# Optimization experiments

Measured on AMD Instinct MI355X. Metric: run time of the kernel, lower is better.

## Reference

```python
import jax, jax.numpy as jnp
import numpy as np

D = 128
N_DATA = 100000
N_TASK = 20000
E = 1000000


def _conv_params(key, d):
    ks = jax.random.split(key, 9)
    s = 1.0 / np.sqrt(d)
    return dict(
        Wmn=jax.random.uniform(ks[0], (d, d), jnp.float32, -s, s),
        bmn=jnp.zeros((d,), jnp.float32),
        Wme=jax.random.uniform(ks[1], (d, 1), jnp.float32, -1.0, 1.0),
        bme=jnp.zeros((d,), jnp.float32),
        Wgn=jax.random.uniform(ks[2], (d, d), jnp.float32, -s, s),
        bgn=jnp.zeros((d,), jnp.float32),
        Wge=jax.random.uniform(ks[3], (d, 1), jnp.float32, -1.0, 1.0),
        bge=jnp.zeros((d,), jnp.float32),
        bias=jnp.zeros((d,), jnp.float32),  # HeteConvLayer bias, zeros-init
    )


def setup_inputs() -> dict:
    key = jax.random.key(0)
    ks = jax.random.split(key, 12)
    inp = {
        'x_data': jax.random.normal(ks[0], (N_DATA, D), jnp.float32),
        'x_task': jax.random.normal(ks[1], (N_TASK, D), jnp.float32),
        'src_dt': jax.random.randint(ks[2], (E,), 0, N_DATA, jnp.int32),
        'dst_dt': jax.random.randint(ks[3], (E,), 0, N_TASK, jnp.int32),
        'ef_dt': jax.random.uniform(ks[4], (E, 1), jnp.float32),
        'src_td': jax.random.randint(ks[5], (E,), 0, N_TASK, jnp.int32),
        'dst_td': jax.random.randint(ks[6], (E,), 0, N_DATA, jnp.int32),
        'ef_td': jax.random.uniform(ks[7], (E, 1), jnp.float32),
    }
    # two separate HeteConvLayers (cfg.kg.hete=True)
    for name, k in (('dt', ks[8]), ('td', ks[9])):
        for pn, pv in _conv_params(k, D).items():
            inp[pn + '_' + name] = pv
    s = 1.0 / np.sqrt(D)
    inp['Ws_data'] = jax.random.uniform(ks[10], (D, D), jnp.float32, -s, s)
    inp['bs_data'] = jnp.zeros((D,), jnp.float32)
    inp['Ws_task'] = jax.random.uniform(ks[11], (D, D), jnp.float32, -s, s)
    inp['bs_task'] = jnp.zeros((D,), jnp.float32)
    return inp


def _hete_conv(x_neigh, src, dst, ef, Wmn, bmn, Wme, bme, Wgn, bgn, Wge, bge, bias, n_out):
    xj = x_neigh[src]                                   # [E, D] gather
    msg = xj @ Wmn.T + bmn + ef @ Wme.T + bme           # [E, D]
    gate = jax.nn.sigmoid(xj @ Wgn.T + bgn + ef @ Wge.T + bge) - 0.5  # gate_bias
    msg = msg * gate
    return jax.ops.segment_sum(msg, dst, num_segments=n_out) + bias


def _self_layer(x, Ws, bs):
    return (jax.nn.sigmoid(x @ Ws.T + bs) + 0.5) * x    # SelfLayer, gate_bias=True


def reference(x_data, x_task, src_dt, dst_dt, ef_dt, src_td, dst_td, ef_td,
              Wmn_dt, bmn_dt, Wme_dt, bme_dt, Wgn_dt, bgn_dt, Wge_dt, bge_dt, bias_dt,
              Wmn_td, bmn_td, Wme_td, bme_td, Wgn_td, bgn_td, Wge_td, bge_td, bias_td,
              Ws_data, bs_data, Ws_task, bs_task):
    # message type (data, property, task): neigh=data, self=task
    agg_task = _hete_conv(x_data, src_dt, dst_dt, ef_dt,
                          Wmn_dt, bmn_dt, Wme_dt, bme_dt,
                          Wgn_dt, bgn_dt, Wge_dt, bge_dt, bias_dt, N_TASK)
    # message type (task, property, data): neigh=task, self=data
    agg_data = _hete_conv(x_task, src_td, dst_td, ef_td,
                          Wmn_td, bmn_td, Wme_td, bme_td,
                          Wgn_td, bgn_td, Wge_td, bge_td, bias_td, N_DATA)
    # add self-transform, aggr='add', then Postlayer = ReLU
    data_emb = jax.nn.relu(agg_data + _self_layer(x_data, Ws_data, bs_data))
    task_emb = jax.nn.relu(agg_task + _self_layer(x_task, Ws_task, bs_task))
    # concatenate node-type outputs along node axis for a single output array
    return jnp.concatenate([data_emb, task_emb], axis=0)
```

## Files before the change

kernel.cpp:

```cpp
#include <hip/hip_runtime.h>
#include <hip/hip_bf16.h>
#include <cstdint>
#include <cstddef>

#define D_DIM 128
#define NEG_LOG2E (-1.44269504f)

typedef __attribute__((ext_vector_type(8))) short short8;
typedef __attribute__((ext_vector_type(4))) float f32x4;

__device__ __forceinline__ float sigmoid_fast(float z) {
  return __builtin_amdgcn_rcpf(1.0f + __expf(-z));
}

__device__ __forceinline__ unsigned short f2bf(float f) {
  union { float f; unsigned u; } v; v.f = f;
  unsigned r = v.u + 0x7FFF + ((v.u >> 16) & 1);
  return (unsigned short)(r >> 16);
}
__device__ __forceinline__ float bf_lo(unsigned u) { return __uint_as_float(u << 16); }
__device__ __forceinline__ float bf_hi(unsigned u) { return __uint_as_float(u & 0xFFFF0000u); }

__global__ __launch_bounds__(256) void fused_pre_kernel(
    const float* __restrict__ s0, const float* __restrict__ s1, const float* __restrict__ s2,
    const float* __restrict__ s3, const float* __restrict__ s4, const float* __restrict__ s5,
    short* __restrict__ wdst,
    const int* __restrict__ dst_dt, const int* __restrict__ dst_td,
    int* __restrict__ ghist, int* __restrict__ done,
    int* __restrict__ bbase, int* __restrict__ bcur, int* __restrict__ offsets,
    int nbt, int NB, int E, int n_tot) {
  __shared__ int lh[768];
  __shared__ int sc[256];
  __shared__ int lastflag;
  int t = threadIdx.x;

  if (blockIdx.x < 96) {
    int idx = blockIdx.x * 256 + t;
    int mat = idx >> 12;
    int pos = (idx & 4095) * 4;
    const float* s = (mat == 0) ? s0 : (mat == 1) ? s1 : (mat == 2) ? s2
                   : (mat == 3) ? s3 : (mat == 4) ? s4 : s5;
    float4 f = *(const float4*)(s + pos);
    short4 o;
    o.x = (short)f2bf(f.x); o.y = (short)f2bf(f.y);
    o.z = (short)f2bf(f.z); o.w = (short)f2bf(f.w);
    *(short4*)(wdst + mat * 16384 + pos) = o;
  }

  lh[t] = 0; lh[t + 256] = 0; lh[t + 512] = 0;
  __syncthreads();
  for (int i = blockIdx.x * 256 + t; i < E; i += gridDim.x * 256) {
    atomicAdd(&lh[dst_dt[i] >> 6], 1);
    atomicAdd(&lh[nbt + (dst_td[i] >> 8)], 1);
  }
  __syncthreads();
#pragma unroll
  for (int k = 0; k < 3; ++k) {
    int b = t + k * 256;
    int c = lh[b];
    if (b < NB && c) atomicAdd(&ghist[b], c);
  }
  __threadfence();
  __syncthreads();
  if (t == 0) {
    int prev = atomicAdd(done, 1);
    lastflag = (prev == (int)gridDim.x - 1);
  }
  __syncthreads();
  if (!lastflag) return;
  __threadfence();

  int i0 = t * 3;
  int c0 = (i0     < NB) ? atomicAdd(&ghist[i0],     0) : 0;
  int c1 = (i0 + 1 < NB) ? atomicAdd(&ghist[i0 + 1], 0) : 0;
  int c2 = (i0 + 2 < NB) ? atomicAdd(&ghist[i0 + 2], 0) : 0;
  int tot = c0 + c1 + c2;
  sc[t] = tot; __syncthreads();
  for (int s = 1; s < 256; s <<= 1) {
    int u = (t >= s) ? sc[t - s] : 0;
    __syncthreads(); sc[t] += u; __syncthreads();
  }
  int base = sc[t] - tot;
  if (i0     < NB) { bbase[i0]     = base;           bcur[i0]     = base; }
  if (i0 + 1 < NB) { bbase[i0 + 1] = base + c0;      bcur[i0 + 1] = base + c0; }
  if (i0 + 2 < NB) { bbase[i0 + 2] = base + c0 + c1; bcur[i0 + 2] = base + c0 + c1; }
  if (t == 255) { bbase[NB] = sc[255]; offsets[n_tot] = sc[255]; }
}

__global__ __launch_bounds__(256) void node_mfma_all(
    const float* __restrict__ x_data, const float* __restrict__ x_task,
    const short* __restrict__ Wb,
    const float* __restrict__ bmn_dt, const float* __restrict__ bme_dt,
    const float* __restrict__ bgn_dt, const float* __restrict__ bge_dt,
    const float* __restrict__ bmn_td, const float* __restrict__ bme_td,
    const float* __restrict__ bgn_td, const float* __restrict__ bge_td,
    const float* __restrict__ bs_data, const float* __restrict__ bs_task,
    const float* __restrict__ bias_dt, const float* __restrict__ bias_td,
    unsigned int* __restrict__ YG_dt, unsigned int* __restrict__ YG_td,
    float* __restrict__ out, int n_data, int n_task, int gd) {
  __shared__ unsigned sh[32][132];
  const bool is_data = (int)blockIdx.x < gd;
  const float* x; const short *Wmnb, *Wgnb, *Wsb;
  const float *bmn, *bme, *bgn, *bge, *bs, *bias_other;
  unsigned* YG; float* out_init; int n, bid;
  if (is_data) {
    x = x_data; Wmnb = Wb; Wgnb = Wb + 16384; Wsb = Wb + 32768;
    bmn = bmn_dt; bme = bme_dt; bgn = bgn_dt; bge = bge_dt;
    bs = bs_data; bias_other = bias_td;
    YG = YG_dt; out_init = out; n = n_data; bid = blockIdx.x;
  } else {
    x = x_task; Wmnb = Wb + 3 * 16384; Wgnb = Wb + 4 * 16384; Wsb = Wb + 5 * 16384;
    bmn = bmn_td; bme = bme_td; bgn = bgn_td; bge = bge_td;
    bs = bs_task; bias_other = bias_dt;
    YG = YG_td; out_init = out + (size_t)n_data * D_DIM; n = n_task; bid = blockIdx.x - gd;
  }
  const int t = threadIdx.x;
  const int wave = t >> 6, lane = t & 63;
  const int q = lane >> 4, l15 = lane & 15;
  const int ng = wave >> 1;
  const int h = (wave & 1) * 64;
  const int base_node = bid * 32;
  const int node_base = base_node + ng * 16;

  short8 a[4];
  {
    int m = node_base + l15;
    int mc = m < n ? m : (n - 1);
    const float* xrow = x + (size_t)mc * D_DIM;
#pragma unroll
    for (int ks = 0; ks < 4; ++ks) {
      float4 f0 = *(const float4*)(xrow + ks * 32 + q * 8);
      float4 f1 = *(const float4*)(xrow + ks * 32 + q * 8 + 4);
      union { short8 s; __hip_bfloat162 hh[4]; } u;
      u.hh[0] = __float22bfloat162_rn({f0.x, f0.y});
      u.hh[1] = __float22bfloat162_rn({f0.z, f0.w});
      u.hh[2] = __float22bfloat162_rn({f1.x, f1.y});
      u.hh[3] = __float22bfloat162_rn({f1.z, f1.w});
      a[ks] = u.s;
    }
  }

  f32x4 accY[4], accG[4], accS[4];
#pragma unroll
  for (int nt = 0; nt < 4; ++nt) { accY[nt] = {0,0,0,0}; accG[nt] = {0,0,0,0}; accS[nt] = {0,0,0,0}; }

#pragma unroll
  for (int nt = 0; nt < 4; ++nt) {
    const int row = h + nt * 16 + l15;
#pragma unroll
    for (int ks = 0; ks < 4; ++ks) {
      const int off = row * D_DIM + ks * 32 + q * 8;
      short8 bm  = *(const short8*)(Wmnb + off);
      short8 bg  = *(const short8*)(Wgnb + off);
      short8 bsw = *(const short8*)(Wsb + off);
      accY[nt] = __builtin_amdgcn_mfma_f32_16x16x32_bf16(a[ks], bm,  accY[nt], 0, 0, 0);
      accG[nt] = __builtin_amdgcn_mfma_f32_16x16x32_bf16(a[ks], bg,  accG[nt], 0, 0, 0);
      accS[nt] = __builtin_amdgcn_mfma_f32_16x16x32_bf16(a[ks], bsw, accS[nt], 0, 0, 0);
    }
  }

#pragma unroll
  for (int nt = 0; nt < 4; ++nt) {
    int d = h + nt * 16 + l15;
    float bmv = bmn[d] + bme[d];
    float bgv = bgn[d] + bge[d];
#pragma unroll
    for (int r = 0; r < 4; ++r) {
      union { __hip_bfloat162 hh; unsigned u; } pck;
      pck.hh = __float22bfloat162_rn({accY[nt][r] + bmv,
                                      (accG[nt][r] + bgv) * NEG_LOG2E});
      sh[ng * 16 + q * 4 + r][d] = pck.u;
    }
  }
  __syncthreads();
#pragma unroll
  for (int it = 0; it < 4; ++it) {
    int idx = (it * 256 + t) * 4;
    int nl = idx >> 7, dd = idx & 127;
    int node = base_node + nl;
    if (node < n)
      *(uint4*)(YG + (size_t)node * D_DIM + dd) = *(const uint4*)&sh[nl][dd];
  }
  __syncthreads();

  float* shf = (float*)sh;
#pragma unroll
  for (int nt = 0; nt < 4; ++nt) {
    int d = h + nt * 16 + l15;
    float bsv = bs[d];
#pragma unroll
    for (int r = 0; r < 4; ++r)
      shf[(ng * 16 + q * 4 + r) * 132 + d] = sigmoid_fast(accS[nt][r] + bsv) + 0.5f;
  }
  __syncthreads();
#pragma unroll
  for (int it = 0; it < 4; ++it) {
    int idx = (it * 256 + t) * 4;
    int nl = idx >> 7, dd = idx & 127;
    int node = base_node + nl;
    if (node < n) {
      float4 xv = *(const float4*)(x + (size_t)node * D_DIM + dd);
      float4 bo = *(const float4*)(bias_other + dd);
      const float* sp = &shf[nl * 132 + dd];
      float4 o;
      o.x = sp[0] * xv.x + bo.x;
      o.y = sp[1] * xv.y + bo.y;
      o.z = sp[2] * xv.z + bo.z;
      o.w = sp[3] * xv.w + bo.w;
      *(float4*)(out_init + (size_t)node * D_DIM + dd) = o;
    }
  }
}

__global__ __launch_bounds__(256) void sort_a_kernel(
    const int* __restrict__ src_dt, const int* __restrict__ dst_dt, const float* __restrict__ ef_dt,
    const int* __restrict__ src_td, const int* __restrict__ dst_td, const float* __restrict__ ef_td,
    int* __restrict__ bcur, int2* __restrict__ eA, int nbt, int NB, int E) {
  __shared__ int lh[768];
  __shared__ int lcur[768];
  int t = threadIdx.x;
  lh[t] = 0; lh[t + 256] = 0; lh[t + 512] = 0;
  __syncthreads();
  int e0 = blockIdx.x * 4096;
  int e1 = min(E, e0 + 4096);
  for (int i = e0 + t; i < e1; i += 256) {
    atomicAdd(&lh[dst_dt[i] >> 6], 1);
    atomicAdd(&lh[nbt + (dst_td[i] >> 8)], 1);
  }
  __syncthreads();
#pragma unroll
  for (int k = 0; k < 3; ++k) {
    int b = t + k * 256;
    int c = lh[b];
    if (b < NB && c) lcur[b] = atomicAdd(&bcur[b], c);
  }
  __syncthreads();
  for (int i = e0 + t; i < e1; i += 256) {
    int c = dst_dt[i];
    int bkt = c >> 6;
    int pos = atomicAdd(&lcur[bkt], 1);
    eA[pos] = make_int2(src_dt[i],
        (int)((__float_as_uint(ef_dt[i]) & 0xFFFFFF00u) | (unsigned)(c & 63)));
    int cd = dst_td[i];
    int bkt2 = nbt + (cd >> 8);
    int pos2 = atomicAdd(&lcur[bkt2], 1);
    eA[pos2] = make_int2(src_td[i],
        (int)((__float_as_uint(ef_td[i]) & 0xFFFFFF00u) | (unsigned)(cd & 255)));
  }
}

__global__ __launch_bounds__(256) void sort_b_kernel(
    const int2* __restrict__ eA, const int* __restrict__ bbase,
    int* __restrict__ offsets, int2* __restrict__ eB,
    int nbt, int n_task, int n_tot) {
  __shared__ int lh[256], sc[256], lcur[256];
  int b = blockIdx.x, t = threadIdx.x;
  int base = bbase[b];
  int cnt = bbase[b + 1] - base;
  int c0, nloc;
  if (b < nbt) { c0 = b << 6; nloc = min(64, n_task - c0); }
  else { c0 = n_task + ((b - nbt) << 8); nloc = min(256, n_tot - c0); }
  lh[t] = 0; __syncthreads();
  for (int i = base + t; i < base + cnt; i += 256)
    atomicAdd(&lh[((unsigned)eA[i].y) & 255u], 1);
  __syncthreads();
  int v = lh[t];
  sc[t] = v; __syncthreads();
  for (int s = 1; s < 256; s <<= 1) {
    int u = (t >= s) ? sc[t - s] : 0;
    __syncthreads(); sc[t] += u; __syncthreads();
  }
  int ex = sc[t] - v;
  lcur[t] = base + ex;
  if (t < nloc) offsets[c0 + t] = base + ex;
  __syncthreads();
  for (int i = base + t; i < base + cnt; i += 256) {
    int2 e = eA[i];
    int pos = atomicAdd(&lcur[((unsigned)e.y) & 255u], 1);
    eB[pos] = e;
  }
}

__device__ __forceinline__ void gstep(float2& acc, int2 e, const unsigned* __restrict__ YG,
                                      int lane, float2 wme, float2 wge2) {
  uint2 yg = *(const uint2*)(YG + (size_t)e.x * D_DIM + 2 * lane);
  float f = __int_as_float(e.y & (int)0xFFFFFF00);
  float g0 = __builtin_amdgcn_rcpf(1.0f + __builtin_amdgcn_exp2f(fmaf(f, wge2.x, bf_hi(yg.x)))) - 0.5f;
  float g1 = __builtin_amdgcn_rcpf(1.0f + __builtin_amdgcn_exp2f(fmaf(f, wge2.y, bf_hi(yg.y)))) - 0.5f;
  acc.x = fmaf(fmaf(f, wme.x, bf_lo(yg.x)), g0, acc.x);
  acc.y = fmaf(fmaf(f, wme.y, bf_lo(yg.y)), g1, acc.y);
}

__global__ __launch_bounds__(256) void gather_kernel(
    const unsigned* __restrict__ YG_dt, const unsigned* __restrict__ YG_td,
    const int* __restrict__ offsets, const int2* __restrict__ edata,
    const float* __restrict__ Wme_dt, const float* __restrict__ Wge_dt,
    const float* __restrict__ Wme_td, const float* __restrict__ Wge_td,
    float* __restrict__ out, int n_task, int n_data) {
  int w = (int)((blockIdx.x * 256u + threadIdx.x) >> 6);
  int lane = threadIdx.x & 63;
  if (w >= n_task + n_data) return;
  bool is_dt = w < n_task;
  const unsigned* YG = is_dt ? YG_dt : YG_td;
  const float* Wme = is_dt ? Wme_dt : Wme_td;
  const float* Wge = is_dt ? Wge_dt : Wge_td;
  size_t orow = is_dt ? (size_t)(n_data + w) : (size_t)(w - n_task);
  int beg = __builtin_amdgcn_readfirstlane(offsets[w]);
  int end = __builtin_amdgcn_readfirstlane(offsets[w + 1]);
  float2 wme = *(const float2*)(Wme + 2 * lane);
  float2 wge = *(const float2*)(Wge + 2 * lane);
  float2 wge2 = {wge.x * NEG_LOG2E, wge.y * NEG_LOG2E};
  float* op = out + orow * D_DIM + 2 * lane;
  float2 acc0 = *(const float2*)op;
  float2 acc1 = {0.0f, 0.0f};
  int p = beg;
  for (; p + 8 <= end; p += 8) {
    int2 e0 = edata[p],     e1 = edata[p + 1], e2 = edata[p + 2], e3 = edata[p + 3];
    int2 e4 = edata[p + 4], e5 = edata[p + 5], e6 = edata[p + 6], e7 = edata[p + 7];
    gstep(acc0, e0, YG, lane, wme, wge2);
    gstep(acc1, e1, YG, lane, wme, wge2);
    gstep(acc0, e2, YG, lane, wme, wge2);
    gstep(acc1, e3, YG, lane, wme, wge2);
    gstep(acc0, e4, YG, lane, wme, wge2);
    gstep(acc1, e5, YG, lane, wme, wge2);
    gstep(acc0, e6, YG, lane, wme, wge2);
    gstep(acc1, e7, YG, lane, wme, wge2);
  }
  for (; p + 2 <= end; p += 2) {
    int2 e0 = edata[p], e1 = edata[p + 1];
    gstep(acc0, e0, YG, lane, wme, wge2);
    gstep(acc1, e1, YG, lane, wme, wge2);
  }
  if (p < end) gstep(acc0, edata[p], YG, lane, wme, wge2);
  acc0.x = fmaxf(acc0.x + acc1.x, 0.0f);
  acc0.y = fmaxf(acc0.y + acc1.y, 0.0f);
  *(float2*)op = acc0;
}

extern "C" void kernel_launch(void* const* d_in, const int* in_sizes, int n_in,
                              void* d_out, int out_size, void* d_ws, size_t ws_size,
                              hipStream_t stream) {
  const float* x_data  = (const float*)d_in[0];
  const float* x_task  = (const float*)d_in[1];
  const int*   src_dt  = (const int*)d_in[2];
  const int*   dst_dt  = (const int*)d_in[3];
  const float* ef_dt   = (const float*)d_in[4];
  const int*   src_td  = (const int*)d_in[5];
  const int*   dst_td  = (const int*)d_in[6];
  const float* ef_td   = (const float*)d_in[7];
  const float* Wmn_dt  = (const float*)d_in[8];
  const float* bmn_dt  = (const float*)d_in[9];
  const float* Wme_dt  = (const float*)d_in[10];
  const float* bme_dt  = (const float*)d_in[11];
  const float* Wgn_dt  = (const float*)d_in[12];
  const float* bgn_dt  = (const float*)d_in[13];
  const float* Wge_dt  = (const float*)d_in[14];
  const float* bge_dt  = (const float*)d_in[15];
  const float* bias_dt = (const float*)d_in[16];
  const float* Wmn_td  = (const float*)d_in[17];
  const float* bmn_td  = (const float*)d_in[18];
  const float* Wme_td  = (const float*)d_in[19];
  const float* bme_td  = (const float*)d_in[20];
  const float* Wgn_td  = (const float*)d_in[21];
  const float* bgn_td  = (const float*)d_in[22];
  const float* Wge_td  = (const float*)d_in[23];
  const float* bge_td  = (const float*)d_in[24];
  const float* bias_td = (const float*)d_in[25];
  const float* Ws_data = (const float*)d_in[26];
  const float* bs_data = (const float*)d_in[27];
  const float* Ws_task = (const float*)d_in[28];
  const float* bs_task = (const float*)d_in[29];
  float* out = (float*)d_out;

  const int N_DATA = in_sizes[0] / D_DIM;
  const int N_TASK = in_sizes[1] / D_DIM;
  const int E = in_sizes[2];
  const int N_TOT = N_TASK + N_DATA;
  const int NBT = (N_TASK + 63) >> 6;
  const int NBD = (N_DATA + 255) >> 8;
  const int NB = NBT + NBD;
  const int GD = (N_DATA + 31) / 32;
  const int GT = (N_TASK + 31) / 32;

  char* ws = (char*)d_ws;
  size_t off = 0;
  auto alloc = [&](size_t bytes) { void* p = ws + off; off += (bytes + 255) & ~(size_t)255; return p; };
  unsigned int* YG_dt = (unsigned int*)alloc((size_t)N_DATA * D_DIM * 4);
  unsigned int* YG_td = (unsigned int*)alloc((size_t)N_TASK * D_DIM * 4);
  int2* eA     = (int2*)alloc((size_t)2 * E * 8);
  int2* eB     = (int2*)alloc((size_t)2 * E * 8);
  int*  offs   = (int*)alloc((size_t)(N_TOT + 1) * 4);
  int*  ghist  = (int*)alloc(1024 * 4);
  int*  bbase  = (int*)alloc(768 * 4);
  int*  bcur   = (int*)alloc(768 * 4);
  short* Wb    = (short*)alloc((size_t)6 * 16384 * 2);
  (void)ws_size; (void)n_in; (void)out_size;

  hipMemsetAsync(ghist, 0, 1024 * 4, stream);

  fused_pre_kernel<<<256, 256, 0, stream>>>(
      Wmn_dt, Wgn_dt, Ws_data, Wmn_td, Wgn_td, Ws_task, Wb,
      dst_dt, dst_td, ghist, ghist + 768, bbase, bcur, offs,
      NBT, NB, E, N_TOT);

  node_mfma_all<<<GD + GT, 256, 0, stream>>>(
      x_data, x_task, Wb,
      bmn_dt, bme_dt, bgn_dt, bge_dt,
      bmn_td, bme_td, bgn_td, bge_td,
      bs_data, bs_task, bias_dt, bias_td,
      YG_dt, YG_td, out, N_DATA, N_TASK, GD);

  sort_a_kernel<<<(E + 4095) / 4096, 256, 0, stream>>>(
      src_dt, dst_dt, ef_dt, src_td, dst_td, ef_td, bcur, eA, NBT, NB, E);
  sort_b_kernel<<<NB, 256, 0, stream>>>(eA, bbase, offs, eB, NBT, N_TASK, N_TOT);

  gather_kernel<<<(N_TOT + 3) / 4, 256, 0, stream>>>(
      YG_dt, YG_td, offs, eB, Wme_dt, Wge_dt, Wme_td, Wge_td, out, N_TASK, N_DATA);
}
```

Before: 492.0 us.

## Replace second sort pass with per-bucket LDS atomic accumulation gather

Drops the second counting-sort pass that ordered edges by exact destination node. Data-side buckets shrink from 256 to 64 nodes, and a new bucket-level gather kernel accumulates gated messages into a 64x128 LDS tile with shared-memory float atomics, then applies ReLU and writes out. This removes one full read and write of the edge array plus the per-node offsets, at the cost of many LDS atomics and a 32KB LDS footprint per block, which may limit occupancy.

```diff
diff --git a/kernel.cpp b/kernel.cpp
--- a/kernel.cpp
+++ b/kernel.cpp
@@ -27,9 +27,9 @@
     short* __restrict__ wdst,
     const int* __restrict__ dst_dt, const int* __restrict__ dst_td,
     int* __restrict__ ghist, int* __restrict__ done,
-    int* __restrict__ bbase, int* __restrict__ bcur, int* __restrict__ offsets,
-    int nbt, int NB, int E, int n_tot) {
-  __shared__ int lh[768];
+    int* __restrict__ bbase, int* __restrict__ bcur,
+    int nbt, int NB, int E) {
+  __shared__ int lh[2048];
   __shared__ int sc[256];
   __shared__ int lastflag;
   int t = threadIdx.x;
@@ -47,15 +47,16 @@
     *(short4*)(wdst + mat * 16384 + pos) = o;
   }
 
-  lh[t] = 0; lh[t + 256] = 0; lh[t + 512] = 0;
+#pragma unroll
+  for (int k = 0; k < 8; ++k) lh[t + k * 256] = 0;
   __syncthreads();
   for (int i = blockIdx.x * 256 + t; i < E; i += gridDim.x * 256) {
     atomicAdd(&lh[dst_dt[i] >> 6], 1);
-    atomicAdd(&lh[nbt + (dst_td[i] >> 8)], 1);
-  }
-  __syncthreads();
-#pragma unroll
-  for (int k = 0; k < 3; ++k) {
+    atomicAdd(&lh[nbt + (dst_td[i] >> 6)], 1);
+  }
+  __syncthreads();
+#pragma unroll
+  for (int k = 0; k < 8; ++k) {
     int b = t + k * 256;
     int c = lh[b];
     if (b < NB && c) atomicAdd(&ghist[b], c);
@@ -70,21 +71,24 @@
   if (!lastflag) return;
   __threadfence();
 
-  int i0 = t * 3;
-  int c0 = (i0     < NB) ? atomicAdd(&ghist[i0],     0) : 0;
-  int c1 = (i0 + 1 < NB) ? atomicAdd(&ghist[i0 + 1], 0) : 0;
-  int c2 = (i0 + 2 < NB) ? atomicAdd(&ghist[i0 + 2], 0) : 0;
-  int tot = c0 + c1 + c2;
-  sc[t] = tot; __syncthreads();
-  for (int s = 1; s < 256; s <<= 1) {
-    int u = (t >= s) ? sc[t - s] : 0;
+  int i0 = t * 8;
+  int c[8]; int s = 0;
+#pragma unroll
+  for (int k = 0; k < 8; ++k) {
+    c[k] = (i0 + k < NB) ? atomicAdd(&ghist[i0 + k], 0) : 0;
+    s += c[k];
+  }
+  sc[t] = s; __syncthreads();
+  for (int st = 1; st < 256; st <<= 1) {
+    int u = (t >= st) ? sc[t - st] : 0;
     __syncthreads(); sc[t] += u; __syncthreads();
   }
-  int base = sc[t] - tot;
-  if (i0     < NB) { bbase[i0]     = base;           bcur[i0]     = base; }
-  if (i0 + 1 < NB) { bbase[i0 + 1] = base + c0;      bcur[i0 + 1] = base + c0; }
-  if (i0 + 2 < NB) { bbase[i0 + 2] = base + c0 + c1; bcur[i0 + 2] = base + c0 + c1; }
-  if (t == 255) { bbase[NB] = sc[255]; offsets[n_tot] = sc[255]; }
+  int base = sc[t] - s;
+#pragma unroll
+  for (int k = 0; k < 8; ++k) {
+    if (i0 + k < NB) { bbase[i0 + k] = base; bcur[i0 + k] = base; base += c[k]; }
+  }
+  if (t == 255) bbase[NB] = sc[255];
 }
 
 __global__ __launch_bounds__(256) void node_mfma_all(
@@ -216,20 +220,21 @@
     const int* __restrict__ src_dt, const int* __restrict__ dst_dt, const float* __restrict__ ef_dt,
     const int* __restrict__ src_td, const int* __restrict__ dst_td, const float* __restrict__ ef_td,
     int* __restrict__ bcur, int2* __restrict__ eA, int nbt, int NB, int E) {
-  __shared__ int lh[768];
-  __shared__ int lcur[768];
+  __shared__ int lh[2048];
+  __shared__ int lcur[2048];
   int t = threadIdx.x;
-  lh[t] = 0; lh[t + 256] = 0; lh[t + 512] = 0;
+#pragma unroll
+  for (int k = 0; k < 8; ++k) lh[t + k * 256] = 0;
   __syncthreads();
   int e0 = blockIdx.x * 4096;
   int e1 = min(E, e0 + 4096);
   for (int i = e0 + t; i < e1; i += 256) {
     atomicAdd(&lh[dst_dt[i] >> 6], 1);
-    atomicAdd(&lh[nbt + (dst_td[i] >> 8)], 1);
-  }
-  __syncthreads();
-#pragma unroll
-  for (int k = 0; k < 3; ++k) {
+    atomicAdd(&lh[nbt + (dst_td[i] >> 6)], 1);
+  }
+  __syncthreads();
+#pragma unroll
+  for (int k = 0; k < 8; ++k) {
     int b = t + k * 256;
     int c = lh[b];
     if (b < NB && c) lcur[b] = atomicAdd(&bcur[b], c);
@@ -237,104 +242,72 @@
   __syncthreads();
   for (int i = e0 + t; i < e1; i += 256) {
     int c = dst_dt[i];
-    int bkt = c >> 6;
-    int pos = atomicAdd(&lcur[bkt], 1);
+    int pos = atomicAdd(&lcur[c >> 6], 1);
     eA[pos] = make_int2(src_dt[i],
         (int)((__float_as_uint(ef_dt[i]) & 0xFFFFFF00u) | (unsigned)(c & 63)));
     int cd = dst_td[i];
-    int bkt2 = nbt + (cd >> 8);
-    int pos2 = atomicAdd(&lcur[bkt2], 1);
+    int pos2 = atomicAdd(&lcur[nbt + (cd >> 6)], 1);
     eA[pos2] = make_int2(src_td[i],
-        (int)((__float_as_uint(ef_td[i]) & 0xFFFFFF00u) | (unsigned)(cd & 255)));
-  }
-}
-
-__global__ __launch_bounds__(256) void sort_b_kernel(
-    const int2* __restrict__ eA, const int* __restrict__ bbase,
-    int* __restrict__ offsets, int2* __restrict__ eB,
-    int nbt, int n_task, int n_tot) {
-  __shared__ int lh[256], sc[256], lcur[256];
-  int b = blockIdx.x, t = threadIdx.x;
-  int base = bbase[b];
-  int cnt = bbase[b + 1] - base;
-  int c0, nloc;
-  if (b < nbt) { c0 = b << 6; nloc = min(64, n_task - c0); }
-  else { c0 = n_task + ((b - nbt) << 8); nloc = min(256, n_tot - c0); }
-  lh[t] = 0; __syncthreads();
-  for (int i = base + t; i < base + cnt; i += 256)
-    atomicAdd(&lh[((unsigned)eA[i].y) & 255u], 1);
-  __syncthreads();
-  int v = lh[t];
-  sc[t] = v; __syncthreads();
-  for (int s = 1; s < 256; s <<= 1) {
-    int u = (t >= s) ? sc[t - s] : 0;
-    __syncthreads(); sc[t] += u; __syncthreads();
-  }
-  int ex = sc[t] - v;
-  lcur[t] = base + ex;
-  if (t < nloc) offsets[c0 + t] = base + ex;
-  __syncthreads();
-  for (int i = base + t; i < base + cnt; i += 256) {
-    int2 e = eA[i];
-    int pos = atomicAdd(&lcur[((unsigned)e.y) & 255u], 1);
-    eB[pos] = e;
-  }
-}
-
-__device__ __forceinline__ void gstep(float2& acc, int2 e, const unsigned* __restrict__ YG,
-                                      int lane, float2 wme, float2 wge2) {
-  uint2 yg = *(const uint2*)(YG + (size_t)e.x * D_DIM + 2 * lane);
-  float f = __int_as_float(e.y & (int)0xFFFFFF00);
-  float g0 = __builtin_amdgcn_rcpf(1.0f + __builtin_amdgcn_exp2f(fmaf(f, wge2.x, bf_hi(yg.x)))) - 0.5f;
-  float g1 = __builtin_amdgcn_rcpf(1.0f + __builtin_amdgcn_exp2f(fmaf(f, wge2.y, bf_hi(yg.y)))) - 0.5f;
-  acc.x = fmaf(fmaf(f, wme.x, bf_lo(yg.x)), g0, acc.x);
-  acc.y = fmaf(fmaf(f, wme.y, bf_lo(yg.y)), g1, acc.y);
-}
-
-__global__ __launch_bounds__(256) void gather_kernel(
+        (int)((__float_as_uint(ef_td[i]) & 0xFFFFFF00u) | (unsigned)(cd & 63)));
+  }
+}
+
+__global__ __launch_bounds__(256) void bucket_gather_kernel(
     const unsigned* __restrict__ YG_dt, const unsigned* __restrict__ YG_td,
-    const int* __restrict__ offsets, const int2* __restrict__ edata,
+    const int* __restrict__ bbase, const int2* __restrict__ eA,
     const float* __restrict__ Wme_dt, const float* __restrict__ Wge_dt,
     const float* __restrict__ Wme_td, const float* __restrict__ Wge_td,
-    float* __restrict__ out, int n_task, int n_data) {
-  int w = (int)((blockIdx.x * 256u + threadIdx.x) >> 6);
-  int lane = threadIdx.x & 63;
-  if (w >= n_task + n_data) return;
-  bool is_dt = w < n_task;
-  const unsigned* YG = is_dt ? YG_dt : YG_td;
-  const float* Wme = is_dt ? Wme_dt : Wme_td;
-  const float* Wge = is_dt ? Wge_dt : Wge_td;
-  size_t orow = is_dt ? (size_t)(n_data + w) : (size_t)(w - n_task);
-  int beg = __builtin_amdgcn_readfirstlane(offsets[w]);
-  int end = __builtin_amdgcn_readfirstlane(offsets[w + 1]);
+    float* __restrict__ out, int nbt, int n_task, int n_data) {
+  __shared__ float acc[64][D_DIM];
+  const int b = blockIdx.x, t = threadIdx.x;
+  const bool is_task = b < nbt;
+  const unsigned* YG = is_task ? YG_dt : YG_td;
+  const float* Wme = is_task ? Wme_dt : Wme_td;
+  const float* Wge = is_task ? Wge_dt : Wge_td;
+  int nloc; size_t orow0;
+  if (is_task) { int c0 = b << 6; nloc = min(64, n_task - c0); orow0 = (size_t)(n_data + c0); }
+  else         { int c0 = (b - nbt) << 6; nloc = min(64, n_data - c0); orow0 = (size_t)c0; }
+  float* outp = out + orow0 * D_DIM;
+  for (int i = t; i < (nloc << 5); i += 256) {
+    int r = i >> 5, cI = (i & 31) << 2;
+    *(float4*)&acc[r][cI] = *(const float4*)(outp + r * D_DIM + cI);
+  }
+  const int base = bbase[b], end = bbase[b + 1];
+  const int lane = t & 63, wave = t >> 6;
   float2 wme = *(const float2*)(Wme + 2 * lane);
   float2 wge = *(const float2*)(Wge + 2 * lane);
   float2 wge2 = {wge.x * NEG_LOG2E, wge.y * NEG_LOG2E};
-  float* op = out + orow * D_DIM + 2 * lane;
-  float2 acc0 = *(const float2*)op;
-  float2 acc1 = {0.0f, 0.0f};
-  int p = beg;
-  for (; p + 8 <= end; p += 8) {
-    int2 e0 = edata[p],     e1 = edata[p + 1], e2 = edata[p + 2], e3 = edata[p + 3];
-    int2 e4 = edata[p + 4], e5 = edata[p + 5], e6 = edata[p + 6], e7 = edata[p + 7];
-    gstep(acc0, e0, YG, lane, wme, wge2);
-    gstep(acc1, e1, YG, lane, wme, wge2);
-    gstep(acc0, e2, YG, lane, wme, wge2);
-    gstep(acc1, e3, YG, lane, wme, wge2);
-    gstep(acc0, e4, YG, lane, wme, wge2);
-    gstep(acc1, e5, YG, lane, wme, wge2);
-    gstep(acc0, e6, YG, lane, wme, wge2);
-    gstep(acc1, e7, YG, lane, wme, wge2);
-  }
-  for (; p + 2 <= end; p += 2) {
-    int2 e0 = edata[p], e1 = edata[p + 1];
-    gstep(acc0, e0, YG, lane, wme, wge2);
-    gstep(acc1, e1, YG, lane, wme, wge2);
-  }
-  if (p < end) gstep(acc0, edata[p], YG, lane, wme, wge2);
-  acc0.x = fmaxf(acc0.x + acc1.x, 0.0f);
-  acc0.y = fmaxf(acc0.y + acc1.y, 0.0f);
-  *(float2*)op = acc0;
+  __syncthreads();
+
+  for (int p = base + (wave << 3); p < end; p += 32) {
+    int lim = end - p; if (lim > 8) lim = 8;
+    int2 e[8];
+#pragma unroll
+    for (int j = 0; j < 8; ++j) if (j < lim) e[j] = eA[p + j];
+    uint2 yg[8];
+#pragma unroll
+    for (int j = 0; j < 8; ++j)
+      if (j < lim) yg[j] = *(const uint2*)(YG + (size_t)e[j].x * D_DIM + 2 * lane);
+#pragma unroll
+    for (int j = 0; j < 8; ++j) if (j < lim) {
+      float f = __int_as_float(e[j].y & (int)0xFFFFFF00);
+      float g0 = __builtin_amdgcn_rcpf(1.0f + __builtin_amdgcn_exp2f(fmaf(f, wge2.x, bf_hi(yg[j].x)))) - 0.5f;
+      float g1 = __builtin_amdgcn_rcpf(1.0f + __builtin_amdgcn_exp2f(fmaf(f, wge2.y, bf_hi(yg[j].y)))) - 0.5f;
+      float m0 = fmaf(f, wme.x, bf_lo(yg[j].x)) * g0;
+      float m1 = fmaf(f, wme.y, bf_lo(yg[j].y)) * g1;
+      int loc = e[j].y & 63;
+      atomicAdd(&acc[loc][2 * lane], m0);
+      atomicAdd(&acc[loc][2 * lane + 1], m1);
+    }
+  }
+  __syncthreads();
+  for (int i = t; i < (nloc << 5); i += 256) {
+    int r = i >> 5, cI = (i & 31) << 2;
+    float4 v = *(const float4*)&acc[r][cI];
+    v.x = fmaxf(v.x, 0.0f); v.y = fmaxf(v.y, 0.0f);
+    v.z = fmaxf(v.z, 0.0f); v.w = fmaxf(v.w, 0.0f);
+    *(float4*)(outp + r * D_DIM + cI) = v;
+  }
 }
 
 extern "C" void kernel_launch(void* const* d_in, const int* in_sizes, int n_in,
@@ -375,9 +348,8 @@
   const int N_DATA = in_sizes[0] / D_DIM;
   const int N_TASK = in_sizes[1] / D_DIM;
   const int E = in_sizes[2];
-  const int N_TOT = N_TASK + N_DATA;
   const int NBT = (N_TASK + 63) >> 6;
-  const int NBD = (N_DATA + 255) >> 8;
+  const int NBD = (N_DATA + 63) >> 6;
   const int NB = NBT + NBD;
   const int GD = (N_DATA + 31) / 32;
   const int GT = (N_TASK + 31) / 32;
@@ -388,20 +360,18 @@
   unsigned int* YG_dt = (unsigned int*)alloc((size_t)N_DATA * D_DIM * 4);
   unsigned int* YG_td = (unsigned int*)alloc((size_t)N_TASK * D_DIM * 4);
   int2* eA     = (int2*)alloc((size_t)2 * E * 8);
-  int2* eB     = (int2*)alloc((size_t)2 * E * 8);
-  int*  offs   = (int*)alloc((size_t)(N_TOT + 1) * 4);
-  int*  ghist  = (int*)alloc(1024 * 4);
-  int*  bbase  = (int*)alloc(768 * 4);
-  int*  bcur   = (int*)alloc(768 * 4);
+  int*  ghist  = (int*)alloc(2560 * 4);
+  int*  bbase  = (int*)alloc(2304 * 4);
+  int*  bcur   = (int*)alloc(2304 * 4);
   short* Wb    = (short*)alloc((size_t)6 * 16384 * 2);
   (void)ws_size; (void)n_in; (void)out_size;
 
-  hipMemsetAsync(ghist, 0, 1024 * 4, stream);
+  hipMemsetAsync(ghist, 0, 2560 * 4, stream);
 
   fused_pre_kernel<<<256, 256, 0, stream>>>(
       Wmn_dt, Wgn_dt, Ws_data, Wmn_td, Wgn_td, Ws_task, Wb,
-      dst_dt, dst_td, ghist, ghist + 768, bbase, bcur, offs,
-      NBT, NB, E, N_TOT);
+      dst_dt, dst_td, ghist, ghist + 2048, bbase, bcur,
+      NBT, NB, E);
 
   node_mfma_all<<<GD + GT, 256, 0, stream>>>(
       x_data, x_task, Wb,
@@ -412,8 +382,8 @@
 
   sort_a_kernel<<<(E + 4095) / 4096, 256, 0, stream>>>(
       src_dt, dst_dt, ef_dt, src_td, dst_td, ef_td, bcur, eA, NBT, NB, E);
-  sort_b_kernel<<<NB, 256, 0, stream>>>(eA, bbase, offs, eB, NBT, N_TASK, N_TOT);
-
-  gather_kernel<<<(N_TOT + 3) / 4, 256, 0, stream>>>(
-      YG_dt, YG_td, offs, eB, Wme_dt, Wge_dt, Wme_td, Wge_td, out, N_TASK, N_DATA);
-}
+
+  bucket_gather_kernel<<<NB, 256, 0, stream>>>(
+      YG_dt, YG_td, bbase, eA, Wme_dt, Wge_dt, Wme_td, Wge_td,
+      out, NBT, N_TASK, N_DATA);
+}
```

Measured after the change: 1.747 ms. +255.2%, slower.

## Replace two-pass bucket sort with per-node counting sort via global atomics

Applied to the files above, without the earlier changes.

Swaps the two-level bucketed edge sort (a coarse bucket histogram, a scatter into buckets, then a per-bucket local sort) for a direct per-destination counting sort. It builds a per-node histogram with global atomics, takes a three-kernel exclusive scan, and scatters edges with global atomic cursors. This drops the intermediate eA buffer and one full pass over the edges. In exchange it issues millions of global atomics, on contended counters for the task nodes (about 50 edges each), and it launches more kernels. The edge feature is now stored at full precision instead of carrying the low-byte destination index.

```diff
diff --git a/kernel.cpp b/kernel.cpp
--- a/kernel.cpp
+++ b/kernel.cpp
@@ -21,19 +21,13 @@
 __device__ __forceinline__ float bf_lo(unsigned u) { return __uint_as_float(u << 16); }
 __device__ __forceinline__ float bf_hi(unsigned u) { return __uint_as_float(u & 0xFFFF0000u); }
 
-__global__ __launch_bounds__(256) void fused_pre_kernel(
+__global__ __launch_bounds__(256) void wconv_hist_kernel(
     const float* __restrict__ s0, const float* __restrict__ s1, const float* __restrict__ s2,
     const float* __restrict__ s3, const float* __restrict__ s4, const float* __restrict__ s5,
     short* __restrict__ wdst,
     const int* __restrict__ dst_dt, const int* __restrict__ dst_td,
-    int* __restrict__ ghist, int* __restrict__ done,
-    int* __restrict__ bbase, int* __restrict__ bcur, int* __restrict__ offsets,
-    int nbt, int NB, int E, int n_tot) {
-  __shared__ int lh[768];
-  __shared__ int sc[256];
-  __shared__ int lastflag;
+    int* __restrict__ cnt, int n_task, int E) {
   int t = threadIdx.x;
-
   if (blockIdx.x < 96) {
     int idx = blockIdx.x * 256 + t;
     int mat = idx >> 12;
@@ -46,45 +40,69 @@
     o.z = (short)f2bf(f.z); o.w = (short)f2bf(f.w);
     *(short4*)(wdst + mat * 16384 + pos) = o;
   }
-
-  lh[t] = 0; lh[t + 256] = 0; lh[t + 512] = 0;
+  int E4 = E >> 2;
+  int i = blockIdx.x * 256 + t;
+  if (i < E4) {
+    int4 a = *(const int4*)(dst_dt + 4 * i);
+    atomicAdd(&cnt[a.x], 1); atomicAdd(&cnt[a.y], 1);
+    atomicAdd(&cnt[a.z], 1); atomicAdd(&cnt[a.w], 1);
+    int4 b = *(const int4*)(dst_td + 4 * i);
+    atomicAdd(&cnt[n_task + b.x], 1); atomicAdd(&cnt[n_task + b.y], 1);
+    atomicAdd(&cnt[n_task + b.z], 1); atomicAdd(&cnt[n_task + b.w], 1);
+  }
+  if (blockIdx.x == 0 && t < (E & 3)) {
+    int j = (E & ~3) + t;
+    atomicAdd(&cnt[dst_dt[j]], 1);
+    atomicAdd(&cnt[n_task + dst_td[j]], 1);
+  }
+}
+
+__global__ __launch_bounds__(256) void scan_p1_kernel(
+    const int* __restrict__ cnt, int* __restrict__ bsum, int n_tot) {
+  __shared__ int red[256];
+  int t = threadIdx.x;
+  int idx = blockIdx.x * 256 + t;
+  red[t] = (idx < n_tot) ? cnt[idx] : 0;
   __syncthreads();
-  for (int i = blockIdx.x * 256 + t; i < E; i += gridDim.x * 256) {
-    atomicAdd(&lh[dst_dt[i] >> 6], 1);
-    atomicAdd(&lh[nbt + (dst_td[i] >> 8)], 1);
-  }
-  __syncthreads();
-#pragma unroll
-  for (int k = 0; k < 3; ++k) {
-    int b = t + k * 256;
-    int c = lh[b];
-    if (b < NB && c) atomicAdd(&ghist[b], c);
-  }
-  __threadfence();
-  __syncthreads();
-  if (t == 0) {
-    int prev = atomicAdd(done, 1);
-    lastflag = (prev == (int)gridDim.x - 1);
-  }
-  __syncthreads();
-  if (!lastflag) return;
-  __threadfence();
-
-  int i0 = t * 3;
-  int c0 = (i0     < NB) ? atomicAdd(&ghist[i0],     0) : 0;
-  int c1 = (i0 + 1 < NB) ? atomicAdd(&ghist[i0 + 1], 0) : 0;
-  int c2 = (i0 + 2 < NB) ? atomicAdd(&ghist[i0 + 2], 0) : 0;
-  int tot = c0 + c1 + c2;
-  sc[t] = tot; __syncthreads();
+  for (int s = 128; s > 0; s >>= 1) {
+    if (t < s) red[t] += red[t + s];
+    __syncthreads();
+  }
+  if (t == 0) bsum[blockIdx.x] = red[0];
+}
+
+__global__ __launch_bounds__(512) void scan_p2_kernel(
+    const int* __restrict__ bsum, int* __restrict__ bpre,
+    int* __restrict__ offs, int SB, int n_tot) {
+  __shared__ int sc[512];
+  int t = threadIdx.x;
+  int v = (t < SB) ? bsum[t] : 0;
+  sc[t] = v; __syncthreads();
+  for (int s = 1; s < 512; s <<= 1) {
+    int u = (t >= s) ? sc[t - s] : 0;
+    __syncthreads(); sc[t] += u; __syncthreads();
+  }
+  if (t < SB) bpre[t] = sc[t] - v;
+  if (t == 511) offs[n_tot] = sc[511];
+}
+
+__global__ __launch_bounds__(256) void scan_p3_kernel(
+    const int* __restrict__ cnt, const int* __restrict__ bpre,
+    int* __restrict__ offs, int* __restrict__ cur, int n_tot) {
+  __shared__ int sc[256];
+  int t = threadIdx.x;
+  int idx = blockIdx.x * 256 + t;
+  int v = (idx < n_tot) ? cnt[idx] : 0;
+  sc[t] = v; __syncthreads();
   for (int s = 1; s < 256; s <<= 1) {
     int u = (t >= s) ? sc[t - s] : 0;
     __syncthreads(); sc[t] += u; __syncthreads();
   }
-  int base = sc[t] - tot;
-  if (i0     < NB) { bbase[i0]     = base;           bcur[i0]     = base; }
-  if (i0 + 1 < NB) { bbase[i0 + 1] = base + c0;      bcur[i0 + 1] = base + c0; }
-  if (i0 + 2 < NB) { bbase[i0 + 2] = base + c0 + c1; bcur[i0 + 2] = base + c0 + c1; }
-  if (t == 255) { bbase[NB] = sc[255]; offsets[n_tot] = sc[255]; }
+  if (idx < n_tot) {
+    int base = bpre[blockIdx.x] + sc[t] - v;
+    offs[idx] = base;
+    cur[idx] = base;
+  }
 }
 
 __global__ __launch_bounds__(256) void node_mfma_all(
@@ -212,79 +230,41 @@
   }
 }
 
-__global__ __launch_bounds__(256) void sort_a_kernel(
+__global__ __launch_bounds__(256) void scatter_kernel(
     const int* __restrict__ src_dt, const int* __restrict__ dst_dt, const float* __restrict__ ef_dt,
     const int* __restrict__ src_td, const int* __restrict__ dst_td, const float* __restrict__ ef_td,
-    int* __restrict__ bcur, int2* __restrict__ eA, int nbt, int NB, int E) {
-  __shared__ int lh[768];
-  __shared__ int lcur[768];
-  int t = threadIdx.x;
-  lh[t] = 0; lh[t + 256] = 0; lh[t + 512] = 0;
-  __syncthreads();
-  int e0 = blockIdx.x * 4096;
-  int e1 = min(E, e0 + 4096);
-  for (int i = e0 + t; i < e1; i += 256) {
-    atomicAdd(&lh[dst_dt[i] >> 6], 1);
-    atomicAdd(&lh[nbt + (dst_td[i] >> 8)], 1);
-  }
-  __syncthreads();
-#pragma unroll
-  for (int k = 0; k < 3; ++k) {
-    int b = t + k * 256;
-    int c = lh[b];
-    if (b < NB && c) lcur[b] = atomicAdd(&bcur[b], c);
-  }
-  __syncthreads();
-  for (int i = e0 + t; i < e1; i += 256) {
-    int c = dst_dt[i];
-    int bkt = c >> 6;
-    int pos = atomicAdd(&lcur[bkt], 1);
-    eA[pos] = make_int2(src_dt[i],
-        (int)((__float_as_uint(ef_dt[i]) & 0xFFFFFF00u) | (unsigned)(c & 63)));
-    int cd = dst_td[i];
-    int bkt2 = nbt + (cd >> 8);
-    int pos2 = atomicAdd(&lcur[bkt2], 1);
-    eA[pos2] = make_int2(src_td[i],
-        (int)((__float_as_uint(ef_td[i]) & 0xFFFFFF00u) | (unsigned)(cd & 255)));
-  }
-}
-
-__global__ __launch_bounds__(256) void sort_b_kernel(
-    const int2* __restrict__ eA, const int* __restrict__ bbase,
-    int* __restrict__ offsets, int2* __restrict__ eB,
-    int nbt, int n_task, int n_tot) {
-  __shared__ int lh[256], sc[256], lcur[256];
-  int b = blockIdx.x, t = threadIdx.x;
-  int base = bbase[b];
-  int cnt = bbase[b + 1] - base;
-  int c0, nloc;
-  if (b < nbt) { c0 = b << 6; nloc = min(64, n_task - c0); }
-  else { c0 = n_task + ((b - nbt) << 8); nloc = min(256, n_tot - c0); }
-  lh[t] = 0; __syncthreads();
-  for (int i = base + t; i < base + cnt; i += 256)
-    atomicAdd(&lh[((unsigned)eA[i].y) & 255u], 1);
-  __syncthreads();
-  int v = lh[t];
-  sc[t] = v; __syncthreads();
-  for (int s = 1; s < 256; s <<= 1) {
-    int u = (t >= s) ? sc[t - s] : 0;
-    __syncthreads(); sc[t] += u; __syncthreads();
-  }
-  int ex = sc[t] - v;
-  lcur[t] = base + ex;
-  if (t < nloc) offsets[c0 + t] = base + ex;
-  __syncthreads();
-  for (int i = base + t; i < base + cnt; i += 256) {
-    int2 e = eA[i];
-    int pos = atomicAdd(&lcur[((unsigned)e.y) & 255u], 1);
-    eB[pos] = e;
+    int* __restrict__ cur, int2* __restrict__ eB, int n_task, int E) {
+  int i = blockIdx.x * 256 + threadIdx.x;
+  int E4 = E >> 2;
+  if (i < E4) {
+    int4 s = *(const int4*)(src_dt + 4 * i);
+    int4 d = *(const int4*)(dst_dt + 4 * i);
+    float4 f = *(const float4*)(ef_dt + 4 * i);
+    int p0 = atomicAdd(&cur[d.x], 1); eB[p0] = make_int2(s.x, __float_as_int(f.x));
+    int p1 = atomicAdd(&cur[d.y], 1); eB[p1] = make_int2(s.y, __float_as_int(f.y));
+    int p2 = atomicAdd(&cur[d.z], 1); eB[p2] = make_int2(s.z, __float_as_int(f.z));
+    int p3 = atomicAdd(&cur[d.w], 1); eB[p3] = make_int2(s.w, __float_as_int(f.w));
+    s = *(const int4*)(src_td + 4 * i);
+    d = *(const int4*)(dst_td + 4 * i);
+    f = *(const float4*)(ef_td + 4 * i);
+    int q0 = atomicAdd(&cur[n_task + d.x], 1); eB[q0] = make_int2(s.x, __float_as_int(f.x));
+    int q1 = atomicAdd(&cur[n_task + d.y], 1); eB[q1] = make_int2(s.y, __float_as_int(f.y));
+    int q2 = atomicAdd(&cur[n_task + d.z], 1); eB[q2] = make_int2(s.z, __float_as_int(f.z));
+    int q3 = atomicAdd(&cur[n_task + d.w], 1); eB[q3] = make_int2(s.w, __float_as_int(f.w));
+  }
+  if (blockIdx.x == 0 && threadIdx.x < (E & 3)) {
+    int j = (E & ~3) + threadIdx.x;
+    int p = atomicAdd(&cur[dst_dt[j]], 1);
+    eB[p] = make_int2(src_dt[j], __float_as_int(ef_dt[j]));
+    int q = atomicAdd(&cur[n_task + dst_td[j]], 1);
+    eB[q] = make_int2(src_td[j], __float_as_int(ef_td[j]));
   }
 }
 
 __device__ __forceinline__ void gstep(float2& acc, int2 e, const unsigned* __restrict__ YG,
                                       int lane, float2 wme, float2 wge2) {
   uint2 yg = *(const uint2*)(YG + (size_t)e.x * D_DIM + 2 * lane);
-  float f = __int_as_float(e.y & (int)0xFFFFFF00);
+  float f = __int_as_float(e.y);
   float g0 = __builtin_amdgcn_rcpf(1.0f + __builtin_amdgcn_exp2f(fmaf(f, wge2.x, bf_hi(yg.x)))) - 0.5f;
   float g1 = __builtin_amdgcn_rcpf(1.0f + __builtin_amdgcn_exp2f(fmaf(f, wge2.y, bf_hi(yg.y)))) - 0.5f;
   acc.x = fmaf(fmaf(f, wme.x, bf_lo(yg.x)), g0, acc.x);
@@ -376,9 +356,7 @@
   const int N_TASK = in_sizes[1] / D_DIM;
   const int E = in_sizes[2];
   const int N_TOT = N_TASK + N_DATA;
-  const int NBT = (N_TASK + 63) >> 6;
-  const int NBD = (N_DATA + 255) >> 8;
-  const int NB = NBT + NBD;
+  const int SB = (N_TOT + 255) / 256;
   const int GD = (N_DATA + 31) / 32;
   const int GT = (N_TASK + 31) / 32;
 
@@ -387,21 +365,24 @@
   auto alloc = [&](size_t bytes) { void* p = ws + off; off += (bytes + 255) & ~(size_t)255; return p; };
   unsigned int* YG_dt = (unsigned int*)alloc((size_t)N_DATA * D_DIM * 4);
   unsigned int* YG_td = (unsigned int*)alloc((size_t)N_TASK * D_DIM * 4);
-  int2* eA     = (int2*)alloc((size_t)2 * E * 8);
-  int2* eB     = (int2*)alloc((size_t)2 * E * 8);
-  int*  offs   = (int*)alloc((size_t)(N_TOT + 1) * 4);
-  int*  ghist  = (int*)alloc(1024 * 4);
-  int*  bbase  = (int*)alloc(768 * 4);
-  int*  bcur   = (int*)alloc(768 * 4);
-  short* Wb    = (short*)alloc((size_t)6 * 16384 * 2);
+  int2* eB    = (int2*)alloc((size_t)2 * E * 8);
+  int*  offs  = (int*)alloc((size_t)(N_TOT + 1) * 4);
+  int*  cur   = (int*)alloc((size_t)N_TOT * 4);
+  int*  cnt   = (int*)alloc((size_t)N_TOT * 4);
+  int*  bsum  = (int*)alloc(512 * 4);
+  int*  bpre  = (int*)alloc(512 * 4);
+  short* Wb   = (short*)alloc((size_t)6 * 16384 * 2);
   (void)ws_size; (void)n_in; (void)out_size;
 
-  hipMemsetAsync(ghist, 0, 1024 * 4, stream);
-
-  fused_pre_kernel<<<256, 256, 0, stream>>>(
+  hipMemsetAsync(cnt, 0, (size_t)N_TOT * 4, stream);
+
+  wconv_hist_kernel<<<1024, 256, 0, stream>>>(
       Wmn_dt, Wgn_dt, Ws_data, Wmn_td, Wgn_td, Ws_task, Wb,
-      dst_dt, dst_td, ghist, ghist + 768, bbase, bcur, offs,
-      NBT, NB, E, N_TOT);
+      dst_dt, dst_td, cnt, N_TASK, E);
+
+  scan_p1_kernel<<<SB, 256, 0, stream>>>(cnt, bsum, N_TOT);
+  scan_p2_kernel<<<1, 512, 0, stream>>>(bsum, bpre, offs, SB, N_TOT);
+  scan_p3_kernel<<<SB, 256, 0, stream>>>(cnt, bpre, offs, cur, N_TOT);
 
   node_mfma_all<<<GD + GT, 256, 0, stream>>>(
       x_data, x_task, Wb,
@@ -410,9 +391,8 @@
       bs_data, bs_task, bias_dt, bias_td,
       YG_dt, YG_td, out, N_DATA, N_TASK, GD);
 
-  sort_a_kernel<<<(E + 4095) / 4096, 256, 0, stream>>>(
-      src_dt, dst_dt, ef_dt, src_td, dst_td, ef_td, bcur, eA, NBT, NB, E);
-  sort_b_kernel<<<NB, 256, 0, stream>>>(eA, bbase, offs, eB, NBT, N_TASK, N_TOT);
+  scatter_kernel<<<1024, 256, 0, stream>>>(
+      src_dt, dst_dt, ef_dt, src_td, dst_td, ef_td, cur, eB, N_TASK, E);
 
   gather_kernel<<<(N_TOT + 3) / 4, 256, 0, stream>>>(
       YG_dt, YG_td, offs, eB, Wme_dt, Wge_dt, Wme_td, Wge_td, out, N_TASK, N_DATA);
```

New measurement: 621.3 us. 26.3% more time.

## Software-pipeline gather loads and vectorize edge index reads in sort kernels

Applied to the files above, without the earlier changes.

The gather kernel now prefetches the next batch of eight edge records and their YG rows while it computes the current batch, and it spreads the sum over four accumulators. The aim is to hide gather latency behind computation. The histogram and sort_a passes now read dst/src/ef as int4/float4 vectors, with a scalar fallback for partial blocks. The trade-off is higher register pressure in the gather kernel, which may lower occupancy.

```diff
diff --git a/kernel.cpp b/kernel.cpp
--- a/kernel.cpp
+++ b/kernel.cpp
@@ -49,9 +49,19 @@
 
   lh[t] = 0; lh[t + 256] = 0; lh[t + 512] = 0;
   __syncthreads();
-  for (int i = blockIdx.x * 256 + t; i < E; i += gridDim.x * 256) {
-    atomicAdd(&lh[dst_dt[i] >> 6], 1);
-    atomicAdd(&lh[nbt + (dst_td[i] >> 8)], 1);
+  int E4 = E >> 2;
+  for (int i = blockIdx.x * 256 + t; i < E4; i += gridDim.x * 256) {
+    int4 a = *(const int4*)(dst_dt + 4 * i);
+    atomicAdd(&lh[a.x >> 6], 1); atomicAdd(&lh[a.y >> 6], 1);
+    atomicAdd(&lh[a.z >> 6], 1); atomicAdd(&lh[a.w >> 6], 1);
+    int4 b = *(const int4*)(dst_td + 4 * i);
+    atomicAdd(&lh[nbt + (b.x >> 8)], 1); atomicAdd(&lh[nbt + (b.y >> 8)], 1);
+    atomicAdd(&lh[nbt + (b.z >> 8)], 1); atomicAdd(&lh[nbt + (b.w >> 8)], 1);
+  }
+  if (blockIdx.x == 0 && t < (E & 3)) {
+    int j = (E & ~3) + t;
+    atomicAdd(&lh[dst_dt[j] >> 6], 1);
+    atomicAdd(&lh[nbt + (dst_td[j] >> 8)], 1);
   }
   __syncthreads();
 #pragma unroll
@@ -223,9 +233,23 @@
   __syncthreads();
   int e0 = blockIdx.x * 4096;
   int e1 = min(E, e0 + 4096);
-  for (int i = e0 + t; i < e1; i += 256) {
-    atomicAdd(&lh[dst_dt[i] >> 6], 1);
-    atomicAdd(&lh[nbt + (dst_td[i] >> 8)], 1);
+  const bool full = (e1 - e0 == 4096);
+  if (full) {
+#pragma unroll
+    for (int k = 0; k < 4; ++k) {
+      int b4 = e0 + (k * 256 + t) * 4;
+      int4 d = *(const int4*)(dst_dt + b4);
+      atomicAdd(&lh[d.x >> 6], 1); atomicAdd(&lh[d.y >> 6], 1);
+      atomicAdd(&lh[d.z >> 6], 1); atomicAdd(&lh[d.w >> 6], 1);
+      int4 d2 = *(const int4*)(dst_td + b4);
+      atomicAdd(&lh[nbt + (d2.x >> 8)], 1); atomicAdd(&lh[nbt + (d2.y >> 8)], 1);
+      atomicAdd(&lh[nbt + (d2.z >> 8)], 1); atomicAdd(&lh[nbt + (d2.w >> 8)], 1);
+    }
+  } else {
+    for (int i = e0 + t; i < e1; i += 256) {
+      atomicAdd(&lh[dst_dt[i] >> 6], 1);
+      atomicAdd(&lh[nbt + (dst_td[i] >> 8)], 1);
+    }
   }
   __syncthreads();
 #pragma unroll
@@ -235,18 +259,37 @@
     if (b < NB && c) lcur[b] = atomicAdd(&bcur[b], c);
   }
   __syncthreads();
-  for (int i = e0 + t; i < e1; i += 256) {
-    int c = dst_dt[i];
-    int bkt = c >> 6;
-    int pos = atomicAdd(&lcur[bkt], 1);
-    eA[pos] = make_int2(src_dt[i],
-        (int)((__float_as_uint(ef_dt[i]) & 0xFFFFFF00u) | (unsigned)(c & 63)));
-    int cd = dst_td[i];
-    int bkt2 = nbt + (cd >> 8);
-    int pos2 = atomicAdd(&lcur[bkt2], 1);
-    eA[pos2] = make_int2(src_td[i],
-        (int)((__float_as_uint(ef_td[i]) & 0xFFFFFF00u) | (unsigned)(cd & 255)));
-  }
+#define PUT_DT(ss, dd, ff) do { \
+    int pos = atomicAdd(&lcur[(dd) >> 6], 1); \
+    eA[pos] = make_int2((ss), (int)((__float_as_uint(ff) & 0xFFFFFF00u) | (unsigned)((dd) & 63))); \
+  } while (0)
+#define PUT_TD(ss, dd, ff) do { \
+    int pos = atomicAdd(&lcur[nbt + ((dd) >> 8)], 1); \
+    eA[pos] = make_int2((ss), (int)((__float_as_uint(ff) & 0xFFFFFF00u) | (unsigned)((dd) & 255))); \
+  } while (0)
+  if (full) {
+#pragma unroll
+    for (int k = 0; k < 4; ++k) {
+      int b4 = e0 + (k * 256 + t) * 4;
+      int4 s = *(const int4*)(src_dt + b4);
+      int4 d = *(const int4*)(dst_dt + b4);
+      float4 f = *(const float4*)(ef_dt + b4);
+      PUT_DT(s.x, d.x, f.x); PUT_DT(s.y, d.y, f.y);
+      PUT_DT(s.z, d.z, f.z); PUT_DT(s.w, d.w, f.w);
+      s = *(const int4*)(src_td + b4);
+      d = *(const int4*)(dst_td + b4);
+      f = *(const float4*)(ef_td + b4);
+      PUT_TD(s.x, d.x, f.x); PUT_TD(s.y, d.y, f.y);
+      PUT_TD(s.z, d.z, f.z); PUT_TD(s.w, d.w, f.w);
+    }
+  } else {
+    for (int i = e0 + t; i < e1; i += 256) {
+      PUT_DT(src_dt[i], dst_dt[i], ef_dt[i]);
+      PUT_TD(src_td[i], dst_td[i], ef_td[i]);
+    }
+  }
+#undef PUT_DT
+#undef PUT_TD
 }
 
 __global__ __launch_bounds__(256) void sort_b_kernel(
@@ -281,14 +324,13 @@
   }
 }
 
-__device__ __forceinline__ void gstep(float2& acc, int2 e, const unsigned* __restrict__ YG,
-                                      int lane, float2 wme, float2 wge2) {
-  uint2 yg = *(const uint2*)(YG + (size_t)e.x * D_DIM + 2 * lane);
+__device__ __forceinline__ void gs(float2& acc, int2 e, uint2 yv,
+                                   float2 wme, float2 wge2) {
   float f = __int_as_float(e.y & (int)0xFFFFFF00);
-  float g0 = __builtin_amdgcn_rcpf(1.0f + __builtin_amdgcn_exp2f(fmaf(f, wge2.x, bf_hi(yg.x)))) - 0.5f;
-  float g1 = __builtin_amdgcn_rcpf(1.0f + __builtin_amdgcn_exp2f(fmaf(f, wge2.y, bf_hi(yg.y)))) - 0.5f;
-  acc.x = fmaf(fmaf(f, wme.x, bf_lo(yg.x)), g0, acc.x);
-  acc.y = fmaf(fmaf(f, wme.y, bf_lo(yg.y)), g1, acc.y);
+  float g0 = __builtin_amdgcn_rcpf(1.0f + __builtin_amdgcn_exp2f(fmaf(f, wge2.x, bf_hi(yv.x)))) - 0.5f;
+  float g1 = __builtin_amdgcn_rcpf(1.0f + __builtin_amdgcn_exp2f(fmaf(f, wge2.y, bf_hi(yv.y)))) - 0.5f;
+  acc.x = fmaf(fmaf(f, wme.x, bf_lo(yv.x)), g0, acc.x);
+  acc.y = fmaf(fmaf(f, wme.y, bf_lo(yv.y)), g1, acc.y);
 }
 
 __global__ __launch_bounds__(256) void gather_kernel(
@@ -312,28 +354,40 @@
   float2 wge2 = {wge.x * NEG_LOG2E, wge.y * NEG_LOG2E};
   float* op = out + orow * D_DIM + 2 * lane;
   float2 acc0 = *(const float2*)op;
-  float2 acc1 = {0.0f, 0.0f};
+  float2 acc1 = {0.0f, 0.0f}, acc2 = {0.0f, 0.0f}, acc3 = {0.0f, 0.0f};
   int p = beg;
-  for (; p + 8 <= end; p += 8) {
+#define YGLD(e) (*(const uint2*)(YG + (size_t)(e).x * D_DIM + 2 * lane))
+  if (p + 8 <= end) {
     int2 e0 = edata[p],     e1 = edata[p + 1], e2 = edata[p + 2], e3 = edata[p + 3];
     int2 e4 = edata[p + 4], e5 = edata[p + 5], e6 = edata[p + 6], e7 = edata[p + 7];
-    gstep(acc0, e0, YG, lane, wme, wge2);
-    gstep(acc1, e1, YG, lane, wme, wge2);
-    gstep(acc0, e2, YG, lane, wme, wge2);
-    gstep(acc1, e3, YG, lane, wme, wge2);
-    gstep(acc0, e4, YG, lane, wme, wge2);
-    gstep(acc1, e5, YG, lane, wme, wge2);
-    gstep(acc0, e6, YG, lane, wme, wge2);
-    gstep(acc1, e7, YG, lane, wme, wge2);
-  }
-  for (; p + 2 <= end; p += 2) {
-    int2 e0 = edata[p], e1 = edata[p + 1];
-    gstep(acc0, e0, YG, lane, wme, wge2);
-    gstep(acc1, e1, YG, lane, wme, wge2);
-  }
-  if (p < end) gstep(acc0, edata[p], YG, lane, wme, wge2);
-  acc0.x = fmaxf(acc0.x + acc1.x, 0.0f);
-  acc0.y = fmaxf(acc0.y + acc1.y, 0.0f);
+    uint2 y0 = YGLD(e0), y1 = YGLD(e1), y2 = YGLD(e2), y3 = YGLD(e3);
+    uint2 y4 = YGLD(e4), y5 = YGLD(e5), y6 = YGLD(e6), y7 = YGLD(e7);
+    p += 8;
+    for (; p + 8 <= end; p += 8) {
+      int2 f0 = edata[p],     f1 = edata[p + 1], f2 = edata[p + 2], f3 = edata[p + 3];
+      int2 f4 = edata[p + 4], f5 = edata[p + 5], f6 = edata[p + 6], f7 = edata[p + 7];
+      uint2 z0 = YGLD(f0), z1 = YGLD(f1), z2 = YGLD(f2), z3 = YGLD(f3);
+      uint2 z4 = YGLD(f4), z5 = YGLD(f5), z6 = YGLD(f6), z7 = YGLD(f7);
+      gs(acc0, e0, y0, wme, wge2); gs(acc1, e1, y1, wme, wge2);
+      gs(acc2, e2, y2, wme, wge2); gs(acc3, e3, y3, wme, wge2);
+      gs(acc0, e4, y4, wme, wge2); gs(acc1, e5, y5, wme, wge2);
+      gs(acc2, e6, y6, wme, wge2); gs(acc3, e7, y7, wme, wge2);
+      e0 = f0; e1 = f1; e2 = f2; e3 = f3; e4 = f4; e5 = f5; e6 = f6; e7 = f7;
+      y0 = z0; y1 = z1; y2 = z2; y3 = z3; y4 = z4; y5 = z5; y6 = z6; y7 = z7;
+    }
+    gs(acc0, e0, y0, wme, wge2); gs(acc1, e1, y1, wme, wge2);
+    gs(acc2, e2, y2, wme, wge2); gs(acc3, e3, y3, wme, wge2);
+    gs(acc0, e4, y4, wme, wge2); gs(acc1, e5, y5, wme, wge2);
+    gs(acc2, e6, y6, wme, wge2); gs(acc3, e7, y7, wme, wge2);
+  }
+  for (; p < end; ++p) {
+    int2 et = edata[p];
+    uint2 yt = YGLD(et);
+    gs(acc0, et, yt, wme, wge2);
+  }
+#undef YGLD
+  acc0.x = fmaxf(acc0.x + acc1.x + acc2.x + acc3.x, 0.0f);
+  acc0.y = fmaxf(acc0.y + acc1.y + acc2.y + acc3.y, 0.0f);
   *(float2*)op = acc0;
 }
 
```

After: 477.1 us. 1.03x faster.
